# Kernel optimization log

Measured on AMD Instinct MI355X. Metric: run time of the kernel, lower is better.

Reference implementation:

```python
import jax, jax.numpy as jnp
import numpy as np

EPS = 1e-10        # matches eps in calculate_jeffreys_similarity
NEG = -1e30        # finite 'masked out' logit (avoids NaN for absent classes)
NORM_EPS = 1e-12   # F.normalize clamp


def setup_inputs() -> dict:
    key = jax.random.key(0)
    k1, k2, k3 = jax.random.split(key, 3)
    B, D, H, W = 4, 256, 256, 256
    C, P = 16, 5
    feature_map = jax.random.normal(k1, (B, D, H, W), dtype=jnp.float32)
    prototypes = jax.random.normal(k2, (C * P, D), dtype=jnp.float32)
    gt_mask = jax.random.randint(k3, (B, H, W), 0, C, dtype=jnp.int32)
    return {
        "feature_map": feature_map,
        "prototypes": prototypes,
        "gt_mask": gt_mask,
        "num_prototypes_per_class": P,
    }


def _loss(feature_map, prototypes, gt_mask, P):
    B, D, H, W = feature_map.shape
    N = H * W
    C = prototypes.shape[0] // P

    # [B, N, D] L2-normalized pixel features (F.normalize, eps=1e-12)
    feats = feature_map.reshape(B, D, N).transpose(0, 2, 1)
    feats = feats / jnp.maximum(jnp.linalg.norm(feats, axis=-1, keepdims=True), NORM_EPS)

    # [C, P, D] L2-normalized prototypes
    protos = prototypes.reshape(C, P, D)
    protos = protos / jnp.maximum(jnp.linalg.norm(protos, axis=-1, keepdims=True), NORM_EPS)

    # per-class pixel membership mask [B, C, N]
    mask = gt_mask.reshape(B, 1, N) == jnp.arange(C, dtype=gt_mask.dtype)[None, :, None]
    present = jnp.any(mask, axis=-1)                        # [B, C]

    # cosine similarities: [B, C, P, N]
    sims = jnp.einsum('bnd,cpd->bcpn', feats, protos)

    m = mask[:, :, None, :]                                 # [B, C, 1, N]
    # first softmax over the pixels of the class (original: softmax(similarities, dim=0))
    s1 = jax.nn.softmax(jnp.where(m, sims, NEG), axis=-1)
    # second softmax applied inside calculate_jeffreys_similarity (over the same gathered pixels)
    s2 = jax.nn.softmax(jnp.where(m, s1, NEG), axis=-1)

    # V = distribution + eps; off-mask positions are exactly eps, and since
    # eps*(log eps - log eps)=0 they contribute nothing to the KL sums below,
    # so summing over all N reproduces the gathered-pixel sum exactly.
    V = jnp.where(m, s2, 0.0) + EPS                          # [B, C, P, N]
    logV = jnp.log(V)

    A = jnp.sum(V * logV, axis=-1)                           # [B, C, P]
    # Bmat[b,c,i,j] = sum_n logV[i] * V[j]
    Bmat = jnp.einsum('bcin,bcjn->bcij', logV, V)
    # KL(V_j || V_i) = A[j] - Bmat[i, j]
    M = A[:, :, None, :] - Bmat                              # [B, C, P, P]
    J = M + jnp.swapaxes(M, -1, -2)                          # Jeffreys divergence (symmetric)
    simmat = jnp.exp(-J)                                     # pairwise similarity

    P_ = simmat.shape[-1]
    triu = jnp.triu(jnp.ones((P_, P_), dtype=simmat.dtype), k=1)
    num_pairs = P_ * (P_ - 1) // 2
    class_sim = jnp.sum(simmat * triu, axis=(-1, -2)) / num_pairs   # [B, C]

    # mean over classes that actually appear in the image; empty image -> 0
    class_sim = jnp.where(present, class_sim, 0.0)
    cnt = jnp.sum(present, axis=-1).astype(class_sim.dtype)          # [B]
    batch_loss = jnp.where(cnt > 0, jnp.sum(class_sim, axis=-1) / jnp.maximum(cnt, 1.0), 0.0)
    return jnp.sum(batch_loss) / B


def reference(feature_map, prototypes, gt_mask, num_prototypes_per_class):
    return _loss(feature_map, prototypes, gt_mask, num_prototypes_per_class)
```

## Files before the change

kernel.cpp:

```cpp
#include <hip/hip_runtime.h>
#include <math.h>

#define BB 4
#define DD 256
#define NN 65536
#define CC 16
#define PP 5
#define CP 80
#define EPSV 1e-10f
#define LPAD 68

#define OFF_PLANE  20480
#define OFF_ACC    (OFF_PLANE + BB * PP * NN)
#define ACC_FLOATS (320 + 320 + 64 + BB * CC * 16)

__global__ void k_norm(const float* __restrict__ protos,
                       float* __restrict__ protosN,
                       float* __restrict__ acc) {
    if (blockIdx.x == CP) {
        for (int i = threadIdx.x; i < ACC_FLOATS; i += 256) acc[i] = 0.f;
        return;
    }
    int r = blockIdx.x;
    int d = threadIdx.x;
    float v = protos[r * DD + d];
    __shared__ float red[256];
    red[d] = v * v;
    __syncthreads();
    for (int s = 128; s > 0; s >>= 1) {
        if (d < s) red[d] += red[d + s];
        __syncthreads();
    }
    float inv = 1.f / fmaxf(sqrtf(red[0]), 1e-12f);
    protosN[r * DD + d] = v * inv;
}

__global__ __launch_bounds__(256) void k_sims(const float* __restrict__ fmap,
                                              const float* __restrict__ protosN,
                                              const int* __restrict__ gt,
                                              float* __restrict__ plane,
                                              float* __restrict__ denom1,
                                              float* __restrict__ cnt) {
    __shared__ __align__(16) float lp[2][CP * LPAD];
    __shared__ float bins[CP];
    __shared__ float binc[CC];
    const int tid = threadIdx.x;
    const int b   = blockIdx.x >> 7;
    const int n0  = ((blockIdx.x & 127) << 9) + (tid << 1);

    if (tid < CP) bins[tid] = 0.f;
    if (tid < CC) binc[tid] = 0.f;

    const int2 cls = *reinterpret_cast<const int2*>(&gt[(size_t)b * NN + n0]);
    const float* fb = fmap + (size_t)b * DD * NN + n0;

    float4 stg[5];
    #pragma unroll
    for (int r = 0; r < 5; ++r) {
        int idx = (r << 8) + tid;
        stg[r] = *reinterpret_cast<const float4*>(
            &protosN[(idx >> 4) * DD + ((idx & 15) << 2)]);
    }
    #pragma unroll
    for (int r = 0; r < 5; ++r) {
        int idx = (r << 8) + tid;
        *reinterpret_cast<float4*>(&lp[0][(idx >> 4) * LPAD + ((idx & 15) << 2)]) = stg[r];
    }
    __syncthreads();

    float dot0[PP] = {0.f, 0.f, 0.f, 0.f, 0.f};
    float dot1[PP] = {0.f, 0.f, 0.f, 0.f, 0.f};
    float nrm0 = 0.f, nrm1 = 0.f;

    for (int ch = 0; ch < 4; ++ch) {
        const int cur = ch & 1;
        if (ch < 3) {
            #pragma unroll
            for (int r = 0; r < 5; ++r) {
                int idx = (r << 8) + tid;
                stg[r] = *reinterpret_cast<const float4*>(
                    &protosN[(idx >> 4) * DD + (ch + 1) * 64 + ((idx & 15) << 2)]);
            }
        }
        const float* lb0 = &lp[cur][cls.x * (PP * LPAD)];
        const float* lb1 = &lp[cur][cls.y * (PP * LPAD)];
        const float* fch = fb + (size_t)(ch * 64) * NN;
        #pragma unroll 2
        for (int dl4 = 0; dl4 < 64; dl4 += 4) {
            float4 pv0[PP], pv1[PP];
            #pragma unroll
            for (int p = 0; p < PP; ++p) {
                pv0[p] = *reinterpret_cast<const float4*>(&lb0[p * LPAD + dl4]);
                pv1[p] = *reinterpret_cast<const float4*>(&lb1[p * LPAD + dl4]);
            }
            #pragma unroll
            for (int k = 0; k < 4; ++k) {
                const float2 f = *reinterpret_cast<const float2*>(&fch[(size_t)(dl4 + k) * NN]);
                nrm0 = fmaf(f.x, f.x, nrm0);
                nrm1 = fmaf(f.y, f.y, nrm1);
                #pragma unroll
                for (int p = 0; p < PP; ++p) {
                    dot0[p] = fmaf(f.x, reinterpret_cast<const float*>(&pv0[p])[k], dot0[p]);
                    dot1[p] = fmaf(f.y, reinterpret_cast<const float*>(&pv1[p])[k], dot1[p]);
                }
            }
        }
        if (ch < 3) {
            #pragma unroll
            for (int r = 0; r < 5; ++r) {
                int idx = (r << 8) + tid;
                *reinterpret_cast<float4*>(
                    &lp[cur ^ 1][(idx >> 4) * LPAD + ((idx & 15) << 2)]) = stg[r];
            }
            __syncthreads();
        }
    }

    const float inv0 = 1.f / fmaxf(sqrtf(nrm0), 1e-12f);
    const float inv1 = 1.f / fmaxf(sqrtf(nrm1), 1e-12f);
    #pragma unroll
    for (int p = 0; p < PP; ++p) {
        float2 e;
        e.x = __expf(dot0[p] * inv0 - 1.f);
        e.y = __expf(dot1[p] * inv1 - 1.f);
        *reinterpret_cast<float2*>(&plane[(size_t)(b * PP + p) * NN + n0]) = e;
        atomicAdd(&bins[cls.x * PP + p], e.x);
        atomicAdd(&bins[cls.y * PP + p], e.y);
    }
    atomicAdd(&binc[cls.x], 1.f);
    atomicAdd(&binc[cls.y], 1.f);
    __syncthreads();
    if (tid < CP) atomicAdd(&denom1[b * CP + tid], bins[tid]);
    if (tid < CC) atomicAdd(&cnt[b * CC + tid], binc[tid]);
}

__global__ __launch_bounds__(256) void k_s2(const int* __restrict__ gt,
                                            float* __restrict__ plane,
                                            const float* __restrict__ denom1,
                                            float* __restrict__ denom2) {
    __shared__ float inv1s[CP];
    __shared__ float bins[4][CP];
    const int tid = threadIdx.x;
    const int w   = tid >> 6;
    const int b   = blockIdx.x >> 6;
    const int n0  = ((blockIdx.x & 63) << 10) + (tid << 2);
    if (tid < CP) inv1s[tid] = 1.f / denom1[b * CP + tid];
    for (int i = tid; i < 4 * CP; i += 256) (&bins[0][0])[i] = 0.f;
    __syncthreads();
    const int4 cls = *reinterpret_cast<const int4*>(&gt[(size_t)b * NN + n0]);
    #pragma unroll
    for (int p = 0; p < PP; ++p) {
        size_t idx = (size_t)(b * PP + p) * NN + n0;
        float4 e = *reinterpret_cast<const float4*>(&plane[idx]);
        float4 u;
        u.x = __expf(e.x * inv1s[cls.x * PP + p] - 1.f);
        u.y = __expf(e.y * inv1s[cls.y * PP + p] - 1.f);
        u.z = __expf(e.z * inv1s[cls.z * PP + p] - 1.f);
        u.w = __expf(e.w * inv1s[cls.w * PP + p] - 1.f);
        *reinterpret_cast<float4*>(&plane[idx]) = u;
        atomicAdd(&bins[w][cls.x * PP + p], u.x);
        atomicAdd(&bins[w][cls.y * PP + p], u.y);
        atomicAdd(&bins[w][cls.z * PP + p], u.z);
        atomicAdd(&bins[w][cls.w * PP + p], u.w);
    }
    __syncthreads();
    if (tid < CP)
        atomicAdd(&denom2[b * CP + tid],
                  bins[0][tid] + bins[1][tid] + bins[2][tid] + bins[3][tid]);
}

__global__ __launch_bounds__(256) void k_bmat(const int* __restrict__ gt,
                                              const float* __restrict__ plane,
                                              const float* __restrict__ denom2,
                                              float* __restrict__ Bbins) {
    __shared__ float inv2s[CP];
    __shared__ float sb[4][CC * 16];
    const int tid = threadIdx.x;
    const int w   = tid >> 6;
    const int b   = blockIdx.x >> 6;
    const int n0  = ((blockIdx.x & 63) << 10) + (tid << 2);
    if (tid < CP) inv2s[tid] = 1.f / denom2[b * CP + tid];
    for (int i = tid; i < 4 * CC * 16; i += 256) (&sb[0][0])[i] = 0.f;
    __syncthreads();
    const int4 cls = *reinterpret_cast<const int4*>(&gt[(size_t)b * NN + n0]);
    const int c4[4] = {cls.x, cls.y, cls.z, cls.w};
    float V[4][PP], L[4][PP];
    #pragma unroll
    for (int p = 0; p < PP; ++p) {
        size_t idx = (size_t)(b * PP + p) * NN + n0;
        float4 u = *reinterpret_cast<const float4*>(&plane[idx]);
        V[0][p] = fmaf(u.x, inv2s[cls.x * PP + p], EPSV);
        V[1][p] = fmaf(u.y, inv2s[cls.y * PP + p], EPSV);
        V[2][p] = fmaf(u.z, inv2s[cls.z * PP + p], EPSV);
        V[3][p] = fmaf(u.w, inv2s[cls.w * PP + p], EPSV);
    }
    #pragma unroll
    for (int q = 0; q < 4; ++q)
        #pragma unroll
        for (int p = 0; p < PP; ++p) L[q][p] = __logf(V[q][p]);
    #pragma unroll
    for (int q = 0; q < 4; ++q) {
        float* base = &sb[w][c4[q] * 16];
        #pragma unroll
        for (int i = 0; i < PP; ++i) atomicAdd(&base[i], L[q][i] * V[q][i]);
        int slot = 5;
        #pragma unroll
        for (int i = 0; i < PP; ++i)
            #pragma unroll
            for (int j = i + 1; j < PP; ++j) {
                atomicAdd(&base[slot], fmaf(L[q][i], V[q][j], L[q][j] * V[q][i]));
                ++slot;
            }
    }
    __syncthreads();
    for (int i = tid; i < CC * 16; i += 256)
        atomicAdd(&Bbins[b * CC * 16 + i], sb[0][i] + sb[1][i] + sb[2][i] + sb[3][i]);
}

__global__ void k_final(const float* __restrict__ Bbins,
                        const float* __restrict__ cnt,
                        float* __restrict__ out) {
    __shared__ float cs[BB * CC];
    __shared__ float pr[BB * CC];
    const int t = threadIdx.x;
    if (t < BB * CC) {
        const float* bb = &Bbins[t * 16];
        float s = 0.f;
        int slot = 5;
        #pragma unroll
        for (int i = 0; i < PP; ++i)
            for (int j = i + 1; j < PP; ++j) {
                float J = bb[i] + bb[j] - bb[slot];
                ++slot;
                s += __expf(-J);
            }
        bool present = cnt[t] > 0.f;
        cs[t] = present ? s * 0.1f : 0.f;
        pr[t] = present ? 1.f : 0.f;
    }
    __syncthreads();
    if (t == 0) {
        float total = 0.f;
        for (int b = 0; b < BB; ++b) {
            float sc = 0.f, np = 0.f;
            for (int c = 0; c < CC; ++c) { sc += cs[b * CC + c]; np += pr[b * CC + c]; }
            total += (np > 0.f) ? sc / np : 0.f;
        }
        out[0] = total / (float)BB;
    }
}

extern "C" void kernel_launch(void* const* d_in, const int* in_sizes, int n_in,
                              void* d_out, int out_size, void* d_ws, size_t ws_size,
                              hipStream_t stream) {
    const float* fmap   = (const float*)d_in[0];
    const float* protos = (const float*)d_in[1];
    const int*   gt     = (const int*)d_in[2];
    float* ws      = (float*)d_ws;
    float* protosN = ws;
    float* plane   = ws + OFF_PLANE;
    float* acc     = ws + OFF_ACC;
    float* denom1  = acc;
    float* denom2  = acc + 320;
    float* cnt     = acc + 640;
    float* Bbins   = acc + 704;
    float* out     = (float*)d_out;

    k_norm <<<CP + 1, 256, 0, stream>>>(protos, protosN, acc);
    k_sims <<<512, 256, 0, stream>>>(fmap, protosN, gt, plane, denom1, cnt);
    k_s2   <<<256, 256, 0, stream>>>(gt, plane, denom1, denom2);
    k_bmat <<<256, 256, 0, stream>>>(gt, plane, denom2, Bbins);
    k_final<<<1, 64, 0, stream>>>(Bbins, cnt, out);
}
```

Measured before the change: 100.4 us.

## Store prototypes as bf16 in shared memory, prefetch features, recompute softmax

The full normalized prototype table is converted to bf16 and kept whole in LDS, which drops the chunked double-buffering and its per-chunk barriers. Feature loads are software-pipelined in groups of eight channels. The second-softmax kernel no longer writes the plane back; the bmat kernel recomputes the first exponential instead, which removes one full plane write. Rounding prototypes to bf16 lowers the precision of the cosine similarities.

Measured after the change: 93.77 us. 6.6% less time.

```diff
diff --git a/kernel.cpp b/kernel.cpp
--- a/kernel.cpp
+++ b/kernel.cpp
@@ -8,11 +8,17 @@
 #define PP 5
 #define CP 80
 #define EPSV 1e-10f
-#define LPAD 68
+#define PITCH 264
 
 #define OFF_PLANE  20480
 #define OFF_ACC    (OFF_PLANE + BB * PP * NN)
 #define ACC_FLOATS (320 + 320 + 64 + BB * CC * 16)
+
+__device__ __forceinline__ unsigned short f2bf(float f) {
+    unsigned int u = __float_as_uint(f);
+    u += 0x7fffu + ((u >> 16) & 1u);
+    return (unsigned short)(u >> 16);
+}
 
 __global__ void k_norm(const float* __restrict__ protos,
                        float* __restrict__ protosN,
@@ -35,13 +41,48 @@
     protosN[r * DD + d] = v * inv;
 }
 
+__device__ __forceinline__ void loadg(const float* __restrict__ fb, int g,
+                                      float2 (&f)[8]) {
+    const float* p = fb + (size_t)g * 8 * NN;
+    #pragma unroll
+    for (int k = 0; k < 8; ++k)
+        f[k] = *reinterpret_cast<const float2*>(p + (size_t)k * NN);
+}
+
+__device__ __forceinline__ void comp(const char* lb0, const char* lb1,
+                                     const float2 (&f)[8], int g,
+                                     float (&d0)[PP], float (&d1)[PP],
+                                     float& n0, float& n1) {
+    uint4 q0[PP], q1[PP];
+    #pragma unroll
+    for (int p = 0; p < PP; ++p) {
+        q0[p] = *reinterpret_cast<const uint4*>(lb0 + p * (PITCH * 2) + g * 16);
+        q1[p] = *reinterpret_cast<const uint4*>(lb1 + p * (PITCH * 2) + g * 16);
+    }
+    #pragma unroll
+    for (int k = 0; k < 8; ++k) {
+        float fx = f[k].x, fy = f[k].y;
+        n0 = fmaf(fx, fx, n0);
+        n1 = fmaf(fy, fy, n1);
+        #pragma unroll
+        for (int p = 0; p < PP; ++p) {
+            unsigned int w0 = (&q0[p].x)[k >> 1];
+            unsigned int w1 = (&q1[p].x)[k >> 1];
+            float a = __uint_as_float((k & 1) ? (w0 & 0xffff0000u) : (w0 << 16));
+            float c = __uint_as_float((k & 1) ? (w1 & 0xffff0000u) : (w1 << 16));
+            d0[p] = fmaf(fx, a, d0[p]);
+            d1[p] = fmaf(fy, c, d1[p]);
+        }
+    }
+}
+
 __global__ __launch_bounds__(256) void k_sims(const float* __restrict__ fmap,
                                               const float* __restrict__ protosN,
                                               const int* __restrict__ gt,
                                               float* __restrict__ plane,
                                               float* __restrict__ denom1,
                                               float* __restrict__ cnt) {
-    __shared__ __align__(16) float lp[2][CP * LPAD];
+    __shared__ __align__(16) unsigned short lp[CP * PITCH];
     __shared__ float bins[CP];
     __shared__ float binc[CC];
     const int tid = threadIdx.x;
@@ -51,69 +92,33 @@
     if (tid < CP) bins[tid] = 0.f;
     if (tid < CC) binc[tid] = 0.f;
 
+    for (int idx = tid; idx < 5120; idx += 256) {
+        int cp = idx >> 6, q = idx & 63;
+        float4 v = *reinterpret_cast<const float4*>(&protosN[(cp << 8) + (q << 2)]);
+        unsigned int u0 = (unsigned int)f2bf(v.x) | ((unsigned int)f2bf(v.y) << 16);
+        unsigned int u1 = (unsigned int)f2bf(v.z) | ((unsigned int)f2bf(v.w) << 16);
+        *reinterpret_cast<uint2*>(reinterpret_cast<char*>(lp) + cp * (PITCH * 2) + (q << 3))
+            = make_uint2(u0, u1);
+    }
+    __syncthreads();
+
     const int2 cls = *reinterpret_cast<const int2*>(&gt[(size_t)b * NN + n0]);
+    const char* lb0 = reinterpret_cast<const char*>(lp) + cls.x * (PP * PITCH * 2);
+    const char* lb1 = reinterpret_cast<const char*>(lp) + cls.y * (PP * PITCH * 2);
     const float* fb = fmap + (size_t)b * DD * NN + n0;
-
-    float4 stg[5];
-    #pragma unroll
-    for (int r = 0; r < 5; ++r) {
-        int idx = (r << 8) + tid;
-        stg[r] = *reinterpret_cast<const float4*>(
-            &protosN[(idx >> 4) * DD + ((idx & 15) << 2)]);
-    }
-    #pragma unroll
-    for (int r = 0; r < 5; ++r) {
-        int idx = (r << 8) + tid;
-        *reinterpret_cast<float4*>(&lp[0][(idx >> 4) * LPAD + ((idx & 15) << 2)]) = stg[r];
-    }
-    __syncthreads();
 
     float dot0[PP] = {0.f, 0.f, 0.f, 0.f, 0.f};
     float dot1[PP] = {0.f, 0.f, 0.f, 0.f, 0.f};
     float nrm0 = 0.f, nrm1 = 0.f;
-
-    for (int ch = 0; ch < 4; ++ch) {
-        const int cur = ch & 1;
-        if (ch < 3) {
-            #pragma unroll
-            for (int r = 0; r < 5; ++r) {
-                int idx = (r << 8) + tid;
-                stg[r] = *reinterpret_cast<const float4*>(
-                    &protosN[(idx >> 4) * DD + (ch + 1) * 64 + ((idx & 15) << 2)]);
-            }
-        }
-        const float* lb0 = &lp[cur][cls.x * (PP * LPAD)];
-        const float* lb1 = &lp[cur][cls.y * (PP * LPAD)];
-        const float* fch = fb + (size_t)(ch * 64) * NN;
-        #pragma unroll 2
-        for (int dl4 = 0; dl4 < 64; dl4 += 4) {
-            float4 pv0[PP], pv1[PP];
-            #pragma unroll
-            for (int p = 0; p < PP; ++p) {
-                pv0[p] = *reinterpret_cast<const float4*>(&lb0[p * LPAD + dl4]);
-                pv1[p] = *reinterpret_cast<const float4*>(&lb1[p * LPAD + dl4]);
-            }
-            #pragma unroll
-            for (int k = 0; k < 4; ++k) {
-                const float2 f = *reinterpret_cast<const float2*>(&fch[(size_t)(dl4 + k) * NN]);
-                nrm0 = fmaf(f.x, f.x, nrm0);
-                nrm1 = fmaf(f.y, f.y, nrm1);
-                #pragma unroll
-                for (int p = 0; p < PP; ++p) {
-                    dot0[p] = fmaf(f.x, reinterpret_cast<const float*>(&pv0[p])[k], dot0[p]);
-                    dot1[p] = fmaf(f.y, reinterpret_cast<const float*>(&pv1[p])[k], dot1[p]);
-                }
-            }
-        }
-        if (ch < 3) {
-            #pragma unroll
-            for (int r = 0; r < 5; ++r) {
-                int idx = (r << 8) + tid;
-                *reinterpret_cast<float4*>(
-                    &lp[cur ^ 1][(idx >> 4) * LPAD + ((idx & 15) << 2)]) = stg[r];
-            }
-            __syncthreads();
-        }
+    float2 fA[8], fB[8];
+
+    loadg(fb, 0, fA);
+    #pragma unroll 1
+    for (int g = 0; g < 32; g += 2) {
+        loadg(fb, g + 1, fB);
+        comp(lb0, lb1, fA, g, dot0, dot1, nrm0, nrm1);
+        if (g < 30) loadg(fb, g + 2, fA);
+        comp(lb0, lb1, fB, g + 1, dot0, dot1, nrm0, nrm1);
     }
 
     const float inv0 = 1.f / fmaxf(sqrtf(nrm0), 1e-12f);
@@ -134,10 +139,10 @@
     if (tid < CC) atomicAdd(&cnt[b * CC + tid], binc[tid]);
 }
 
-__global__ __launch_bounds__(256) void k_s2(const int* __restrict__ gt,
-                                            float* __restrict__ plane,
-                                            const float* __restrict__ denom1,
-                                            float* __restrict__ denom2) {
+__global__ __launch_bounds__(256) void k_denom2(const int* __restrict__ gt,
+                                                const float* __restrict__ plane,
+                                                const float* __restrict__ denom1,
+                                                float* __restrict__ denom2) {
     __shared__ float inv1s[CP];
     __shared__ float bins[4][CP];
     const int tid = threadIdx.x;
@@ -152,16 +157,10 @@
     for (int p = 0; p < PP; ++p) {
         size_t idx = (size_t)(b * PP + p) * NN + n0;
         float4 e = *reinterpret_cast<const float4*>(&plane[idx]);
-        float4 u;
-        u.x = __expf(e.x * inv1s[cls.x * PP + p] - 1.f);
-        u.y = __expf(e.y * inv1s[cls.y * PP + p] - 1.f);
-        u.z = __expf(e.z * inv1s[cls.z * PP + p] - 1.f);
-        u.w = __expf(e.w * inv1s[cls.w * PP + p] - 1.f);
-        *reinterpret_cast<float4*>(&plane[idx]) = u;
-        atomicAdd(&bins[w][cls.x * PP + p], u.x);
-        atomicAdd(&bins[w][cls.y * PP + p], u.y);
-        atomicAdd(&bins[w][cls.z * PP + p], u.z);
-        atomicAdd(&bins[w][cls.w * PP + p], u.w);
+        atomicAdd(&bins[w][cls.x * PP + p], __expf(e.x * inv1s[cls.x * PP + p] - 1.f));
+        atomicAdd(&bins[w][cls.y * PP + p], __expf(e.y * inv1s[cls.y * PP + p] - 1.f));
+        atomicAdd(&bins[w][cls.z * PP + p], __expf(e.z * inv1s[cls.z * PP + p] - 1.f));
+        atomicAdd(&bins[w][cls.w * PP + p], __expf(e.w * inv1s[cls.w * PP + p] - 1.f));
     }
     __syncthreads();
     if (tid < CP)
@@ -171,15 +170,20 @@
 
 __global__ __launch_bounds__(256) void k_bmat(const int* __restrict__ gt,
                                               const float* __restrict__ plane,
+                                              const float* __restrict__ denom1,
                                               const float* __restrict__ denom2,
                                               float* __restrict__ Bbins) {
+    __shared__ float inv1s[CP];
     __shared__ float inv2s[CP];
     __shared__ float sb[4][CC * 16];
     const int tid = threadIdx.x;
     const int w   = tid >> 6;
     const int b   = blockIdx.x >> 6;
     const int n0  = ((blockIdx.x & 63) << 10) + (tid << 2);
-    if (tid < CP) inv2s[tid] = 1.f / denom2[b * CP + tid];
+    if (tid < CP) {
+        inv1s[tid] = 1.f / denom1[b * CP + tid];
+        inv2s[tid] = 1.f / denom2[b * CP + tid];
+    }
     for (int i = tid; i < 4 * CC * 16; i += 256) (&sb[0][0])[i] = 0.f;
     __syncthreads();
     const int4 cls = *reinterpret_cast<const int4*>(&gt[(size_t)b * NN + n0]);
@@ -188,11 +192,11 @@
     #pragma unroll
     for (int p = 0; p < PP; ++p) {
         size_t idx = (size_t)(b * PP + p) * NN + n0;
-        float4 u = *reinterpret_cast<const float4*>(&plane[idx]);
-        V[0][p] = fmaf(u.x, inv2s[cls.x * PP + p], EPSV);
-        V[1][p] = fmaf(u.y, inv2s[cls.y * PP + p], EPSV);
-        V[2][p] = fmaf(u.z, inv2s[cls.z * PP + p], EPSV);
-        V[3][p] = fmaf(u.w, inv2s[cls.w * PP + p], EPSV);
+        float4 e = *reinterpret_cast<const float4*>(&plane[idx]);
+        V[0][p] = fmaf(__expf(e.x * inv1s[cls.x * PP + p] - 1.f), inv2s[cls.x * PP + p], EPSV);
+        V[1][p] = fmaf(__expf(e.y * inv1s[cls.y * PP + p] - 1.f), inv2s[cls.y * PP + p], EPSV);
+        V[2][p] = fmaf(__expf(e.z * inv1s[cls.z * PP + p] - 1.f), inv2s[cls.z * PP + p], EPSV);
+        V[3][p] = fmaf(__expf(e.w * inv1s[cls.w * PP + p] - 1.f), inv2s[cls.w * PP + p], EPSV);
     }
     #pragma unroll
     for (int q = 0; q < 4; ++q)
@@ -266,9 +270,9 @@
     float* Bbins   = acc + 704;
     float* out     = (float*)d_out;
 
-    k_norm <<<CP + 1, 256, 0, stream>>>(protos, protosN, acc);
-    k_sims <<<512, 256, 0, stream>>>(fmap, protosN, gt, plane, denom1, cnt);
-    k_s2   <<<256, 256, 0, stream>>>(gt, plane, denom1, denom2);
-    k_bmat <<<256, 256, 0, stream>>>(gt, plane, denom2, Bbins);
-    k_final<<<1, 64, 0, stream>>>(Bbins, cnt, out);
-}
+    k_norm  <<<CP + 1, 256, 0, stream>>>(protos, protosN, acc);
+    k_sims  <<<512, 256, 0, stream>>>(fmap, protosN, gt, plane, denom1, cnt);
+    k_denom2<<<256, 256, 0, stream>>>(gt, plane, denom1, denom2);
+    k_bmat  <<<256, 256, 0, stream>>>(gt, plane, denom1, denom2, Bbins);
+    k_final <<<1, 64, 0, stream>>>(Bbins, cnt, out);
+}
```
